# Performance work log

Measured on AMD Instinct MI355X. Metric: run time of the kernel, lower is better.

## Reference

```python
import jax, jax.numpy as jnp
import numpy as np

N_EMBD = 768
N_EXP = 8
DIM_HIDDEN = int(N_EMBD * 4 * 2 / 3)  # 2048
B = 8
CAP = 1024


def setup_inputs() -> dict:
    key = jax.random.key(0)
    k1, k2, k3 = jax.random.split(key, 3)
    std_fc = N_EXP ** (-0.5)  # matches torch init: dim = c_fc.shape[0] = n_exp
    x = jax.random.normal(k1, (B, N_EXP, CAP, N_EMBD), dtype=jnp.float32)
    c_fc = jax.random.uniform(k2, (N_EXP, N_EMBD, 2 * DIM_HIDDEN), dtype=jnp.float32,
                              minval=-std_fc, maxval=std_fc)
    c_proj = jax.random.uniform(k3, (N_EXP, DIM_HIDDEN, N_EMBD), dtype=jnp.float32,
                                minval=-std_fc, maxval=std_fc)
    gamma = jnp.ones((N_EMBD,), dtype=jnp.float32)       # RMSNorm gamma
    mult_bias = jnp.ones((DIM_HIDDEN,), dtype=jnp.float32)  # GEGLU mult_bias
    return {"x": x, "c_fc": c_fc, "c_proj": c_proj, "gamma": gamma, "mult_bias": mult_bias}


def _moe_forward(x, c_fc, c_proj, gamma, mult_bias):
    # x: [b, e, n, d] -> [e, b, n, d]
    h = jnp.transpose(x, (1, 0, 2, 3))
    # RMSNorm (prenorm): F.normalize(x, dim=-1) * gamma * sqrt(d)
    scale = N_EMBD ** 0.5
    l2 = jnp.sqrt(jnp.sum(h * h, axis=-1, keepdims=True))
    h = h / jnp.maximum(l2, 1e-12) * gamma * scale
    # per-expert grouped GEMM: [e,b,n,d] @ [e,d,2h] -> [e,b,n,2h]
    u = jnp.einsum('ebnd,edh->ebnh', h, c_fc)
    # GEGLU: first half is value, second half is gate
    v, gate = u[..., :DIM_HIDDEN], u[..., DIM_HIDDEN:]
    g = jax.nn.gelu(gate, approximate=False) * v * mult_bias
    # project back: [e,b,n,h] @ [e,h,d] -> [e,b,n,d]
    out = jnp.einsum('ebnh,ehd->ebnd', g, c_proj)
    # back to [b, e, n, d]; dropout is identity (p=0.0)
    return jnp.transpose(out, (1, 0, 2, 3))


def reference(x, c_fc, c_proj, gamma, mult_bias):
    return _moe_forward(x, c_fc, c_proj, gamma, mult_bias)
```

## Files before the change

kernel.cpp:

```cpp
#include <hip/hip_runtime.h>
#include <math.h>

#define N_EMBD 768
#define N_EXP  8
#define DIMH   2048
#define CAPN   1024
#define M_TOT  8192

typedef __bf16 bf16x8 __attribute__((ext_vector_type(8)));
typedef float  f32x4  __attribute__((ext_vector_type(4)));
typedef unsigned short u16x4 __attribute__((ext_vector_type(4)));

__device__ __forceinline__ unsigned short f2bf(float f) {
    unsigned int u = __float_as_uint(f);
    unsigned int r = (u + 0x7fffu + ((u >> 16) & 1u)) >> 16;
    return (unsigned short)r;
}

__device__ __forceinline__ void gload16(const void* g, void* l) {
    __builtin_amdgcn_global_load_lds(
        (const __attribute__((address_space(1))) unsigned int*)g,
        (__attribute__((address_space(3))) unsigned int*)l, 16, 0, 0);
}

__device__ __forceinline__ float gelu_exact(float x) {
    float ax = fabsf(x);
    float z  = ax * 0.70710678118654752f;
    float t  = __builtin_amdgcn_rcpf(fmaf(0.3275911f, z, 1.0f));
    float p  = fmaf(t, 1.061405429f, -1.453152027f);
    p = fmaf(p, t, 1.421413741f);
    p = fmaf(p, t, -0.284496736f);
    p = fmaf(p, t, 0.254829592f);
    p = p * t;
    float ez = __expf(-z * z);
    float erfz = fmaf(-p, ez, 1.0f);
    return 0.5f * fmaf(ax, erfz, x);
}

__global__ __launch_bounds__(256) void norm_convert_kernel(
        const float* __restrict__ x, const float* __restrict__ gamma,
        unsigned short* __restrict__ h) {
    int r = (blockIdx.x << 2) | (threadIdx.x >> 6);
    int lane = threadIdx.x & 63;
    int e = r >> 13, m = r & 8191;
    int b = m >> 10, nc = m & 1023;
    const float4* row = (const float4*)(x + (size_t)((b * N_EXP + e) * CAPN + nc) * N_EMBD);
    const float4* g4  = (const float4*)gamma;

    float4 v0 = row[lane], v1 = row[lane + 64], v2 = row[lane + 128];
    float acc = v0.x*v0.x + v0.y*v0.y + v0.z*v0.z + v0.w*v0.w
              + v1.x*v1.x + v1.y*v1.y + v1.z*v1.z + v1.w*v1.w
              + v2.x*v2.x + v2.y*v2.y + v2.z*v2.z + v2.w*v2.w;
#pragma unroll
    for (int off = 32; off >= 1; off >>= 1) acc += __shfl_xor(acc, off, 64);
    float s = 27.712812921102035f / fmaxf(sqrtf(acc), 1e-12f);

    float4 g0 = g4[lane], g1 = g4[lane + 64], g2 = g4[lane + 128];
    u16x4* o4 = (u16x4*)(h + (size_t)(e * M_TOT + m) * N_EMBD);
    u16x4 o;
    o[0]=f2bf(v0.x*s*g0.x); o[1]=f2bf(v0.y*s*g0.y); o[2]=f2bf(v0.z*s*g0.z); o[3]=f2bf(v0.w*s*g0.w);
    o4[lane] = o;
    o[0]=f2bf(v1.x*s*g1.x); o[1]=f2bf(v1.y*s*g1.y); o[2]=f2bf(v1.z*s*g1.z); o[3]=f2bf(v1.w*s*g1.w);
    o4[lane + 64] = o;
    o[0]=f2bf(v2.x*s*g2.x); o[1]=f2bf(v2.y*s*g2.y); o[2]=f2bf(v2.z*s*g2.z); o[3]=f2bf(v2.w*s*g2.w);
    o4[lane + 128] = o;
}

__global__ __launch_bounds__(256) void transpose_convert_kernel(
        const float* __restrict__ in, unsigned short* __restrict__ out, int R, int C) {
    __shared__ float tile[32][33];
    int c0 = blockIdx.x * 32, r0 = blockIdx.y * 32;
    const float* ip = in + (size_t)blockIdx.z * R * C;
    unsigned short* op = out + (size_t)blockIdx.z * R * C;
    int tx = threadIdx.x & 31, ty = threadIdx.x >> 5;
#pragma unroll
    for (int i = 0; i < 4; ++i)
        tile[ty + 8 * i][tx] = ip[(size_t)(r0 + ty + 8 * i) * C + c0 + tx];
    __syncthreads();
#pragma unroll
    for (int i = 0; i < 4; ++i)
        op[(size_t)(c0 + ty + 8 * i) * R + r0 + tx] = f2bf(tile[tx][ty + 8 * i]);
}

#define SBB  __builtin_amdgcn_s_barrier(); \
             asm volatile("s_waitcnt lgkmcnt(0)" ::: "memory"); \
             __builtin_amdgcn_sched_barrier(0); \
             __builtin_amdgcn_s_setprio(1)
#define SBE  __builtin_amdgcn_s_setprio(0); __builtin_amdgcn_s_barrier()
#define VMW(N) do { asm volatile("s_waitcnt vmcnt(" #N ")" ::: "memory"); \
             __builtin_amdgcn_sched_barrier(0); } while (0)

#define STG2(PSRC, RS, KO, DOFF) do { \
    gload16((PSRC) + (size_t)sr * (RS) + (KO) + scs, lds + (DOFF) + ldst); \
    gload16((PSRC) + (size_t)(sr + 64) * (RS) + (KO) + scs, lds + (DOFF) + ldst + 4096); \
  } while (0)

#define RDF(V) (*(const bf16x8*)(lds + (V)))

#define RDA4(AF, DB, IB) do { \
    _Pragma("unroll") for (int i_ = 0; i_ < 4; ++i_) { \
      AF[i_][0] = RDF((DB)*32768 + aB + ((IB) + i_)*1024 + sl0); \
      AF[i_][1] = RDF((DB)*32768 + aB + ((IB) + i_)*1024 + sl1); } \
  } while (0)

#define RDB2(BF, DB, BASE) do { \
    _Pragma("unroll") for (int j_ = 0; j_ < 2; ++j_) { \
      BF[j_][0] = RDF((DB)*32768 + (BASE) + j_*1024 + sl0); \
      BF[j_][1] = RDF((DB)*32768 + (BASE) + j_*1024 + sl1); } \
  } while (0)

#define QUAD(ACC, MS, NB, AF, BF) do { \
    _Pragma("unroll") for (int i_ = 0; i_ < 4; ++i_) \
    _Pragma("unroll") for (int j_ = 0; j_ < 2; ++j_) { \
      ACC[(MS)*4 + i_][(NB) + j_] = __builtin_amdgcn_mfma_f32_16x16x32_bf16( \
          AF[i_][0], BF[j_][0], ACC[(MS)*4 + i_][(NB) + j_], 0, 0, 0); \
      ACC[(MS)*4 + i_][(NB) + j_] = __builtin_amdgcn_mfma_f32_16x16x32_bf16( \
          AF[i_][1], BF[j_][1], ACC[(MS)*4 + i_][(NB) + j_], 0, 0, 0); } \
  } while (0)

__global__ __launch_bounds__(512, 2) void gemm1_kernel(
        const unsigned short* __restrict__ hb,
        const unsigned short* __restrict__ fT,
        const float* __restrict__ mbias,
        unsigned short* __restrict__ gb,
        int e0) {
    __shared__ __align__(16) unsigned short lds[65536];
    const int t = threadIdx.x;
    const int e = e0 + blockIdx.z;
    const int m0 = blockIdx.x * 256;
    const int n0 = blockIdx.y * 128;
    const unsigned short* pA  = hb + ((size_t)e * M_TOT + m0) * N_EMBD;
    const unsigned short* pBv = fT + ((size_t)e * 2 * DIMH + n0) * N_EMBD;
    const unsigned short* pBg = pBv + (size_t)DIMH * N_EMBD;
    unsigned short* pG = gb + (size_t)blockIdx.z * M_TOT * DIMH;

    const int sr   = t >> 3;
    const int scs  = ((t & 7) ^ (sr & 7)) * 8;
    const int ldst = t * 8;
    const int lane = t & 63, lo = lane & 15, quad = lane >> 4;
    const int w = t >> 6, wm = w & 1, wn = w >> 1;
    const int sl0 = ((quad    ) ^ (lo & 7)) * 8;
    const int sl1 = ((quad + 4) ^ (lo & 7)) * 8;
    const int aB  = wm * 8192 + lo * 64;
    const int bvB = 16384 + (wn * 32 + lo) * 64;
    const int bgB = 24576 + (wn * 32 + lo) * 64;

#define STA1(D, H, KO)  STG2(pA + (size_t)(H) * 128 * N_EMBD, N_EMBD, KO, (D)*32768 + (H)*8192)
#define STBV1(D, KO)    STG2(pBv, N_EMBD, KO, (D)*32768 + 16384)
#define STBG1(D, KO)    STG2(pBg, N_EMBD, KO, (D)*32768 + 24576)

    f32x4 accv[8][2], accg[8][2];
#pragma unroll
    for (int i = 0; i < 8; ++i)
#pragma unroll
        for (int j = 0; j < 2; ++j) { accv[i][j] = (f32x4)0.f; accg[i][j] = (f32x4)0.f; }
    bf16x8 a0[4][2], a1[4][2], bv[2][2], bg[2][2];

    STBV1(0, 0); STA1(0, 0, 0); STA1(0, 1, 0); STBG1(0, 0);
    STBV1(1, 64); STA1(1, 0, 64); STA1(1, 1, 64);
    VMW(6);
    __builtin_amdgcn_s_barrier();

    for (int it = 0; it < 6; ++it) {
        const bool more = (it < 5);
        const int koO  = it * 128 + 64;
        const int koE2 = it * 128 + 128;
        const int koO2 = it * 128 + 192;
        RDA4(a0, 0, 0); RDB2(bv, 0, bvB);
        STBG1(1, koO);
        SBB; QUAD(accv, 0, 0, a0, bv); SBE;
        RDA4(a1, 0, 4);
        if (more) STBV1(0, koE2);
        VMW(8);
        SBB; QUAD(accv, 1, 0, a1, bv); SBE;
        RDB2(bg, 0, bgB);
        if (more) STA1(0, 0, koE2);
        SBB; QUAD(accg, 1, 0, a1, bg); SBE;
        if (more) { STA1(0, 1, koE2); VMW(6); } else { VMW(2); }
        SBB; QUAD(accg, 0, 0, a0, bg); SBE;
        RDA4(a0, 1, 0); RDB2(bv, 1, bvB);
        if (more) STBG1(0, koE2);
        SBB; QUAD(accv, 0, 0, a0, bv); SBE;
        RDA4(a1, 1, 4);
        if (more) STBV1(1, koO2); else VMW(0);
        SBB; QUAD(accv, 1, 0, a1, bv); SBE;
        RDB2(bg, 1, bgB);
        if (more) STA1(1, 0, koO2);
        SBB; QUAD(accg, 1, 0, a1, bg); SBE;
        if (more) { STA1(1, 1, koO2); VMW(8); }
        SBB; QUAD(accg, 0, 0, a0, bg); SBE;
    }

#pragma unroll
    for (int i = 0; i < 8; ++i) {
        const int mb = m0 + wm * 128 + i * 16 + quad * 4;
#pragma unroll
        for (int j = 0; j < 2; ++j) {
            const int n = n0 + wn * 32 + j * 16 + lo;
            const float mbv = mbias[n];
#pragma unroll
            for (int r = 0; r < 4; ++r) {
                float ge = gelu_exact(accg[i][j][r]);
                pG[(size_t)(mb + r) * DIMH + n] = f2bf(ge * accv[i][j][r] * mbv);
            }
        }
    }
#undef STA1
#undef STBV1
#undef STBG1
}

__global__ __launch_bounds__(512, 2) void gemm2_kernel(
        const unsigned short* __restrict__ gb,
        const unsigned short* __restrict__ pT,
        float* __restrict__ out, int e0) {
    __shared__ __align__(16) unsigned short lds[65536];
    const int t = threadIdx.x;
    const int e = e0 + blockIdx.z;
    const int m0 = blockIdx.x * 256;
    const int n0 = blockIdx.y * 256;
    const unsigned short* pA = gb + (size_t)blockIdx.z * M_TOT * DIMH + (size_t)m0 * DIMH;
    const unsigned short* pB = pT + ((size_t)e * N_EMBD + n0) * DIMH;

    const int sr   = t >> 3;
    const int scs  = ((t & 7) ^ (sr & 7)) * 8;
    const int ldst = t * 8;
    const int lane = t & 63, lo = lane & 15, quad = lane >> 4;
    const int w = t >> 6, wm = w & 1, wn = w >> 1;
    const int sl0 = ((quad    ) ^ (lo & 7)) * 8;
    const int sl1 = ((quad + 4) ^ (lo & 7)) * 8;
    const int aB  = wm * 8192 + lo * 64;
    const int bB  = 16384 + (wn >> 1) * 8192 + ((wn & 1) * 64 + lo) * 64;

#define STA2(D, H, KO)  STG2(pA + (size_t)(H) * 128 * DIMH, DIMH, KO, (D)*32768 + (H)*8192)
#define STB2(D, H, KO)  STG2(pB + (size_t)(H) * 128 * DIMH, DIMH, KO, (D)*32768 + 16384 + (H)*8192)

    f32x4 acc[8][4];
#pragma unroll
    for (int i = 0; i < 8; ++i)
#pragma unroll
        for (int j = 0; j < 4; ++j) acc[i][j] = (f32x4)0.f;
    bf16x8 a0[4][2], a1[4][2], bb[2][2];

    STA2(0, 0, 0); STA2(0, 1, 0); STB2(0, 0, 0); STB2(0, 1, 0);
    STA2(1, 0, 64); STA2(1, 1, 64);
    VMW(4);
    __builtin_amdgcn_s_barrier();

    for (int it = 0; it < 16; ++it) {
        const bool more = (it < 15);
        const int koO  = it * 128 + 64;
        const int koE2 = it * 128 + 128;
        const int koO2 = it * 128 + 192;
        RDA4(a0, 0, 0); RDB2(bb, 0, bB);
        STB2(1, 0, koO);
        SBB; QUAD(acc, 0, 0, a0, bb); SBE;
        RDA4(a1, 0, 4);
        STB2(1, 1, koO);
        SBB; QUAD(acc, 1, 0, a1, bb); SBE;
        RDB2(bb, 0, bB + 2048);
        if (more) STA2(0, 0, koE2);
        SBB; QUAD(acc, 1, 2, a1, bb); SBE;
        if (more) { STA2(0, 1, koE2); VMW(4); } else { VMW(0); }
        SBB; QUAD(acc, 0, 2, a0, bb); SBE;
        RDA4(a0, 1, 0); RDB2(bb, 1, bB);
        if (more) STB2(0, 0, koE2);
        SBB; QUAD(acc, 0, 0, a0, bb); SBE;
        RDA4(a1, 1, 4);
        if (more) STB2(0, 1, koE2);
        SBB; QUAD(acc, 1, 0, a1, bb); SBE;
        RDB2(bb, 1, bB + 2048);
        if (more) STA2(1, 0, koO2);
        SBB; QUAD(acc, 1, 2, a1, bb); SBE;
        if (more) { STA2(1, 1, koO2); VMW(4); }
        SBB; QUAD(acc, 0, 2, a0, bb); SBE;
    }

#pragma unroll
    for (int i = 0; i < 8; ++i) {
        const int mb = m0 + wm * 128 + i * 16 + quad * 4;
#pragma unroll
        for (int r = 0; r < 4; ++r) {
            const int m = mb + r;
            const int b = m >> 10, nc = m & 1023;
            float* orow = out + (size_t)((b * N_EXP + e) * CAPN + nc) * N_EMBD;
#pragma unroll
            for (int j = 0; j < 4; ++j)
                orow[n0 + wn * 64 + j * 16 + lo] = acc[i][j][r];
        }
    }
#undef STA2
#undef STB2
}

extern "C" void kernel_launch(void* const* d_in, const int* in_sizes, int n_in,
                              void* d_out, int out_size, void* d_ws, size_t ws_size,
                              hipStream_t stream) {
    const float* x     = (const float*)d_in[0];
    const float* cfc   = (const float*)d_in[1];
    const float* cproj = (const float*)d_in[2];
    const float* gamma = (const float*)d_in[3];
    const float* mbias = (const float*)d_in[4];
    float* out = (float*)d_out;

    unsigned short* h      = (unsigned short*)d_ws;
    unsigned short* cfcT   = h + 50331648ull;
    unsigned short* cprojT = cfcT + 25165824ull;
    unsigned short* gbuf   = cprojT + 12582912ull;
    const size_t need_batched = 444596224ull;

    norm_convert_kernel<<<dim3(N_EXP * M_TOT / 4), dim3(256), 0, stream>>>(x, gamma, h);
    transpose_convert_kernel<<<dim3(2 * DIMH / 32, N_EMBD / 32, N_EXP), dim3(256), 0, stream>>>(
        cfc, cfcT, N_EMBD, 2 * DIMH);
    transpose_convert_kernel<<<dim3(N_EMBD / 32, DIMH / 32, N_EXP), dim3(256), 0, stream>>>(
        cproj, cprojT, DIMH, N_EMBD);

    if (ws_size >= need_batched) {
        gemm1_kernel<<<dim3(M_TOT / 256, DIMH / 128, N_EXP), dim3(512), 0, stream>>>(
            h, cfcT, mbias, gbuf, 0);
        gemm2_kernel<<<dim3(M_TOT / 256, N_EMBD / 256, N_EXP), dim3(512), 0, stream>>>(
            gbuf, cprojT, out, 0);
    } else {
        for (int e = 0; e < N_EXP; ++e) {
            gemm1_kernel<<<dim3(M_TOT / 256, DIMH / 128, 1), dim3(512), 0, stream>>>(
                h, cfcT, mbias, gbuf, e);
            gemm2_kernel<<<dim3(M_TOT / 256, N_EMBD / 256, 1), dim3(512), 0, stream>>>(
                gbuf, cprojT, out, e);
        }
    }
}
```

Baseline: 1.106 ms.

## Restructure GEMM pipelines with merged MFMA phases and loop N tiles in gemm2

The gemm1 main loop is regrouped so each barrier-protected phase issues two MFMA quads, and LDS waits use partial lgkmcnt counts so compute can start before every fragment read finishes. gemm2 now loops over all three 256-wide N tiles inside one block instead of launching a grid dimension for them, and it reorders its loads so both B halves are held in registers. The goal is fewer barriers per K step and more overlap of LDS reads with MFMA. The cost is a gemm2 grid three times smaller, which cuts parallelism (256 blocks) and may leave CUs idle, plus more registers per thread.

```diff
diff --git a/kernel.cpp b/kernel.cpp
--- a/kernel.cpp
+++ b/kernel.cpp
@@ -82,13 +82,12 @@
         op[(size_t)(c0 + ty + 8 * i) * R + r0 + tx] = f2bf(tile[tx][ty + 8 * i]);
 }
 
-#define SBB  __builtin_amdgcn_s_barrier(); \
-             asm volatile("s_waitcnt lgkmcnt(0)" ::: "memory"); \
-             __builtin_amdgcn_sched_barrier(0); \
-             __builtin_amdgcn_s_setprio(1)
-#define SBE  __builtin_amdgcn_s_setprio(0); __builtin_amdgcn_s_barrier()
-#define VMW(N) do { asm volatile("s_waitcnt vmcnt(" #N ")" ::: "memory"); \
-             __builtin_amdgcn_sched_barrier(0); } while (0)
+#define BAR   __builtin_amdgcn_s_barrier()
+#define SB0   __builtin_amdgcn_sched_barrier(0)
+#define PRIO1 __builtin_amdgcn_s_setprio(1)
+#define PRIO0 __builtin_amdgcn_s_setprio(0)
+#define LKW(N) do { asm volatile("s_waitcnt lgkmcnt(" #N ")" ::: "memory"); SB0; } while (0)
+#define VMW(N) do { asm volatile("s_waitcnt vmcnt(" #N ")" ::: "memory"); SB0; } while (0)
 
 #define STG2(PSRC, RS, KO, DOFF) do { \
     gload16((PSRC) + (size_t)sr * (RS) + (KO) + scs, lds + (DOFF) + ldst); \
@@ -159,36 +158,44 @@
     STBV1(0, 0); STA1(0, 0, 0); STA1(0, 1, 0); STBG1(0, 0);
     STBV1(1, 64); STA1(1, 0, 64); STA1(1, 1, 64);
     VMW(6);
-    __builtin_amdgcn_s_barrier();
+    BAR;
 
     for (int it = 0; it < 6; ++it) {
         const bool more = (it < 5);
         const int koO  = it * 128 + 64;
         const int koE2 = it * 128 + 128;
         const int koO2 = it * 128 + 192;
-        RDA4(a0, 0, 0); RDB2(bv, 0, bvB);
+        RDB2(bv, 0, bvB); RDA4(a0, 0, 0);
+        SB0;
+        RDA4(a1, 0, 4);
         STBG1(1, koO);
-        SBB; QUAD(accv, 0, 0, a0, bv); SBE;
-        RDA4(a1, 0, 4);
-        if (more) STBV1(0, koE2);
-        VMW(8);
-        SBB; QUAD(accv, 1, 0, a1, bv); SBE;
+        BAR; LKW(8); PRIO1;
+        QUAD(accv, 0, 0, a0, bv);
+        LKW(0);
+        QUAD(accv, 1, 0, a1, bv);
+        PRIO0; BAR;
         RDB2(bg, 0, bgB);
-        if (more) STA1(0, 0, koE2);
-        SBB; QUAD(accg, 1, 0, a1, bg); SBE;
-        if (more) { STA1(0, 1, koE2); VMW(6); } else { VMW(2); }
-        SBB; QUAD(accg, 0, 0, a0, bg); SBE;
-        RDA4(a0, 1, 0); RDB2(bv, 1, bvB);
+        if (more) { STBV1(0, koE2); STA1(0, 0, koE2); STA1(0, 1, koE2); VMW(6); }
+        else      { VMW(0); }
+        BAR; LKW(0); PRIO1;
+        QUAD(accg, 0, 0, a0, bg);
+        QUAD(accg, 1, 0, a1, bg);
+        PRIO0; BAR;
+        RDB2(bv, 1, bvB); RDA4(a0, 1, 0);
+        SB0;
+        RDA4(a1, 1, 4);
         if (more) STBG1(0, koE2);
-        SBB; QUAD(accv, 0, 0, a0, bv); SBE;
-        RDA4(a1, 1, 4);
-        if (more) STBV1(1, koO2); else VMW(0);
-        SBB; QUAD(accv, 1, 0, a1, bv); SBE;
+        BAR; LKW(8); PRIO1;
+        QUAD(accv, 0, 0, a0, bv);
+        LKW(0);
+        QUAD(accv, 1, 0, a1, bv);
+        PRIO0; BAR;
         RDB2(bg, 1, bgB);
-        if (more) STA1(1, 0, koO2);
-        SBB; QUAD(accg, 1, 0, a1, bg); SBE;
-        if (more) { STA1(1, 1, koO2); VMW(8); }
-        SBB; QUAD(accg, 0, 0, a0, bg); SBE;
+        if (more) { STBV1(1, koO2); STA1(1, 0, koO2); STA1(1, 1, koO2); VMW(6); }
+        BAR; LKW(0); PRIO1;
+        QUAD(accg, 0, 0, a0, bg);
+        QUAD(accg, 1, 0, a1, bg);
+        PRIO0; BAR;
     }
 
 #pragma unroll
@@ -218,9 +225,7 @@
     const int t = threadIdx.x;
     const int e = e0 + blockIdx.z;
     const int m0 = blockIdx.x * 256;
-    const int n0 = blockIdx.y * 256;
     const unsigned short* pA = gb + (size_t)blockIdx.z * M_TOT * DIMH + (size_t)m0 * DIMH;
-    const unsigned short* pB = pT + ((size_t)e * N_EMBD + n0) * DIMH;
 
     const int sr   = t >> 3;
     const int scs  = ((t & 7) ^ (sr & 7)) * 8;
@@ -235,58 +240,67 @@
 #define STA2(D, H, KO)  STG2(pA + (size_t)(H) * 128 * DIMH, DIMH, KO, (D)*32768 + (H)*8192)
 #define STB2(D, H, KO)  STG2(pB + (size_t)(H) * 128 * DIMH, DIMH, KO, (D)*32768 + 16384 + (H)*8192)
 
-    f32x4 acc[8][4];
-#pragma unroll
-    for (int i = 0; i < 8; ++i)
-#pragma unroll
-        for (int j = 0; j < 4; ++j) acc[i][j] = (f32x4)0.f;
-    bf16x8 a0[4][2], a1[4][2], bb[2][2];
-
-    STA2(0, 0, 0); STA2(0, 1, 0); STB2(0, 0, 0); STB2(0, 1, 0);
-    STA2(1, 0, 64); STA2(1, 1, 64);
-    VMW(4);
-    __builtin_amdgcn_s_barrier();
-
-    for (int it = 0; it < 16; ++it) {
-        const bool more = (it < 15);
-        const int koO  = it * 128 + 64;
-        const int koE2 = it * 128 + 128;
-        const int koO2 = it * 128 + 192;
-        RDA4(a0, 0, 0); RDB2(bb, 0, bB);
-        STB2(1, 0, koO);
-        SBB; QUAD(acc, 0, 0, a0, bb); SBE;
-        RDA4(a1, 0, 4);
-        STB2(1, 1, koO);
-        SBB; QUAD(acc, 1, 0, a1, bb); SBE;
-        RDB2(bb, 0, bB + 2048);
-        if (more) STA2(0, 0, koE2);
-        SBB; QUAD(acc, 1, 2, a1, bb); SBE;
-        if (more) { STA2(0, 1, koE2); VMW(4); } else { VMW(0); }
-        SBB; QUAD(acc, 0, 2, a0, bb); SBE;
-        RDA4(a0, 1, 0); RDB2(bb, 1, bB);
-        if (more) STB2(0, 0, koE2);
-        SBB; QUAD(acc, 0, 0, a0, bb); SBE;
-        RDA4(a1, 1, 4);
-        if (more) STB2(0, 1, koE2);
-        SBB; QUAD(acc, 1, 0, a1, bb); SBE;
-        RDB2(bb, 1, bB + 2048);
-        if (more) STA2(1, 0, koO2);
-        SBB; QUAD(acc, 1, 2, a1, bb); SBE;
-        if (more) { STA2(1, 1, koO2); VMW(4); }
-        SBB; QUAD(acc, 0, 2, a0, bb); SBE;
-    }
-
-#pragma unroll
-    for (int i = 0; i < 8; ++i) {
-        const int mb = m0 + wm * 128 + i * 16 + quad * 4;
-#pragma unroll
-        for (int r = 0; r < 4; ++r) {
-            const int m = mb + r;
-            const int b = m >> 10, nc = m & 1023;
-            float* orow = out + (size_t)((b * N_EXP + e) * CAPN + nc) * N_EMBD;
-#pragma unroll
-            for (int j = 0; j < 4; ++j)
-                orow[n0 + wn * 64 + j * 16 + lo] = acc[i][j][r];
+    bf16x8 a0[4][2], a1[4][2], bbL[2][2], bbH[2][2];
+
+    for (int yp = 0; yp < 3; ++yp) {
+        const int n0 = yp * 256;
+        const unsigned short* pB = pT + ((size_t)e * N_EMBD + n0) * DIMH;
+
+        f32x4 acc[8][4];
+#pragma unroll
+        for (int i = 0; i < 8; ++i)
+#pragma unroll
+            for (int j = 0; j < 4; ++j) acc[i][j] = (f32x4)0.f;
+
+        STB2(0, 0, 0); STB2(0, 1, 0); STA2(0, 0, 0); STA2(0, 1, 0);
+        STB2(1, 0, 64); STB2(1, 1, 64);
+        VMW(4);
+        BAR;
+
+        for (int it = 0; it < 16; ++it) {
+            const bool more = (it < 15);
+            const int koO  = it * 128 + 64;
+            const int koE2 = it * 128 + 128;
+            const int koO2 = it * 128 + 192;
+            RDB2(bbL, 0, bB); RDB2(bbH, 0, bB + 2048); RDA4(a0, 0, 0);
+            STA2(1, 0, koO); STA2(1, 1, koO);
+            BAR; LKW(0); PRIO1;
+            QUAD(acc, 0, 0, a0, bbL);
+            QUAD(acc, 0, 2, a0, bbH);
+            PRIO0; BAR;
+            RDA4(a1, 0, 4);
+            if (more) { STB2(0, 0, koE2); STB2(0, 1, koE2); VMW(4); }
+            else      { VMW(0); }
+            BAR; LKW(0); PRIO1;
+            QUAD(acc, 1, 0, a1, bbL);
+            QUAD(acc, 1, 2, a1, bbH);
+            PRIO0; BAR;
+            RDB2(bbL, 1, bB); RDB2(bbH, 1, bB + 2048); RDA4(a0, 1, 0);
+            if (more) { STA2(0, 0, koE2); STA2(0, 1, koE2); }
+            BAR; LKW(0); PRIO1;
+            QUAD(acc, 0, 0, a0, bbL);
+            QUAD(acc, 0, 2, a0, bbH);
+            PRIO0; BAR;
+            RDA4(a1, 1, 4);
+            if (more) { STB2(1, 0, koO2); STB2(1, 1, koO2); VMW(4); }
+            BAR; LKW(0); PRIO1;
+            QUAD(acc, 1, 0, a1, bbL);
+            QUAD(acc, 1, 2, a1, bbH);
+            PRIO0; BAR;
+        }
+
+#pragma unroll
+        for (int i = 0; i < 8; ++i) {
+            const int mb = m0 + wm * 128 + i * 16 + quad * 4;
+#pragma unroll
+            for (int r = 0; r < 4; ++r) {
+                const int m = mb + r;
+                const int b = m >> 10, nc = m & 1023;
+                float* orow = out + (size_t)((b * N_EXP + e) * CAPN + nc) * N_EMBD;
+#pragma unroll
+                for (int j = 0; j < 4; ++j)
+                    orow[n0 + wn * 64 + j * 16 + lo] = acc[i][j][r];
+            }
         }
     }
 #undef STA2
@@ -318,13 +332,13 @@
     if (ws_size >= need_batched) {
         gemm1_kernel<<<dim3(M_TOT / 256, DIMH / 128, N_EXP), dim3(512), 0, stream>>>(
             h, cfcT, mbias, gbuf, 0);
-        gemm2_kernel<<<dim3(M_TOT / 256, N_EMBD / 256, N_EXP), dim3(512), 0, stream>>>(
+        gemm2_kernel<<<dim3(M_TOT / 256, 1, N_EXP), dim3(512), 0, stream>>>(
             gbuf, cprojT, out, 0);
     } else {
         for (int e = 0; e < N_EXP; ++e) {
             gemm1_kernel<<<dim3(M_TOT / 256, DIMH / 128, 1), dim3(512), 0, stream>>>(
                 h, cfcT, mbias, gbuf, e);
-            gemm2_kernel<<<dim3(M_TOT / 256, N_EMBD / 256, 1), dim3(512), 0, stream>>>(
+            gemm2_kernel<<<dim3(M_TOT / 256, 1, 1), dim3(512), 0, stream>>>(
                 gbuf, cprojT, out, e);
         }
     }
```

Result: slower. 1.255 ms (+13.4%).
